# Kernel optimization log

Hardware: AMD Instinct MI355X
Metric: run time of the kernel (lower is better)

## Reference

```python
import jax, jax.numpy as jnp
import numpy as np

LATENT, HIDDEN = 512, 1024


def _gru_cell(x, h, w_ih, w_hh, b_ih, b_hh):
    # PyTorch GRU cell: gates ordered (r, z, n)
    gi = x @ w_ih.T + b_ih          # (B, 3H)
    gh = h @ w_hh.T + b_hh          # (B, 3H)
    i_r, i_z, i_n = jnp.split(gi, 3, axis=-1)
    h_r, h_z, h_n = jnp.split(gh, 3, axis=-1)
    r = jax.nn.sigmoid(i_r + h_r)
    z = jax.nn.sigmoid(i_z + h_z)
    n = jnp.tanh(i_n + r * h_n)
    return (1.0 - z) * n + z * h


def setup_inputs() -> dict:
    key = jax.random.key(0)
    ks = jax.random.split(key, 16)
    B, T_in = 128, 64
    k = 1.0 / np.sqrt(HIDDEN)
    u = lambda kk, shape: jax.random.uniform(kk, shape, jnp.float32, -k, k)
    return {
        "context_latents": jax.random.normal(ks[0], (B, T_in, LATENT), jnp.float32),
        "w_ih_l0": u(ks[1], (3 * HIDDEN, LATENT)),
        "w_hh_l0": u(ks[2], (3 * HIDDEN, HIDDEN)),
        "b_ih_l0": u(ks[3], (3 * HIDDEN,)),
        "b_hh_l0": u(ks[4], (3 * HIDDEN,)),
        "w_ih_l1": u(ks[5], (3 * HIDDEN, HIDDEN)),
        "w_hh_l1": u(ks[6], (3 * HIDDEN, HIDDEN)),
        "b_ih_l1": u(ks[7], (3 * HIDDEN,)),
        "b_hh_l1": u(ks[8], (3 * HIDDEN,)),
        "w1": u(ks[9], (HIDDEN, HIDDEN)),
        "bp1": u(ks[10], (HIDDEN,)),
        "w2": u(ks[11], (LATENT, HIDDEN)),
        "bp2": u(ks[12], (LATENT,)),
        "num_predictions": 64,
    }


def reference(context_latents, w_ih_l0, w_hh_l0, b_ih_l0, b_hh_l0,
              w_ih_l1, w_hh_l1, b_ih_l1, b_hh_l1, w1, bp1, w2, bp2,
              num_predictions):
    B = context_latents.shape[0]
    h0 = jnp.zeros((B, HIDDEN), context_latents.dtype)
    h1 = jnp.zeros((B, HIDDEN), context_latents.dtype)

    def stack(x_t, h0, h1):
        h0 = _gru_cell(x_t, h0, w_ih_l0, w_hh_l0, b_ih_l0, b_hh_l0)
        h1 = _gru_cell(h0, h1, w_ih_l1, w_hh_l1, b_ih_l1, b_hh_l1)
        return h0, h1

    # Encode context: scan over time (B, T_in, D) -> final hidden states
    def enc_step(carry, x_t):
        h0, h1 = carry
        h0, h1 = stack(x_t, h0, h1)
        return (h0, h1), None

    (h0, h1), _ = jax.lax.scan(enc_step, (h0, h1),
                               jnp.swapaxes(context_latents, 0, 1))

    def dec_step(carry, _):
        h0, h1, x = carry
        h0, h1 = stack(x, h0, h1)
        y = jax.nn.relu(h1 @ w1.T + bp1) @ w2.T + bp2   # (B, LATENT)
        return (h0, h1, y), y

    x0 = context_latents[:, -1, :]
    _, ys = jax.lax.scan(dec_step, (h0, h1, x0), None, length=num_predictions)
    return jnp.swapaxes(ys, 0, 1)  # (B, T_out, LATENT)
```

## Files before the change

kernel.cpp:

```cpp
#include <hip/hip_runtime.h>
#include <math.h>

#define B 128
#define LATENT 512
#define H 1024
#define BH (B * H)

typedef unsigned short ushort_t;
typedef unsigned int uint_t;
typedef __bf16 bf16x8 __attribute__((ext_vector_type(8)));
typedef float f32x4 __attribute__((ext_vector_type(4)));


__global__ __launch_bounds__(256) void zero4_kernel(float4* __restrict__ p, int n4) {
  int i = blockIdx.x * blockDim.x + threadIdx.x;
  int stride = gridDim.x * blockDim.x;
  float4 z = {0.f, 0.f, 0.f, 0.f};
  for (; i < n4; i += stride) p[i] = z;
}

__device__ __forceinline__ void split_bf16(float f, ushort_t& h, ushort_t& l) {
  uint_t u = __float_as_uint(f);
  uint_t hb = (u + 0x7FFFu + ((u >> 16) & 1u)) >> 16;
  float fh = __uint_as_float(hb << 16);
  float r = f - fh;
  uint_t v = __float_as_uint(r);
  uint_t lb = (v + 0x7FFFu + ((v >> 16) & 1u)) >> 16;
  h = (ushort_t)hb; l = (ushort_t)lb;
}

__global__ __launch_bounds__(256) void split_kernel(const float* __restrict__ src,
                                                    ushort_t* __restrict__ hi,
                                                    ushort_t* __restrict__ lo, int n) {
  int i = blockIdx.x * blockDim.x + threadIdx.x;
  int stride = gridDim.x * blockDim.x;
  for (; i < n; i += stride) {
    ushort_t h, l;
    split_bf16(src[i], h, l);
    hi[i] = h; lo[i] = l;
  }
}

__global__ __launch_bounds__(256) void split_hi_kernel(const float* __restrict__ src,
                                                       ushort_t* __restrict__ hi, int n) {
  int i = blockIdx.x * blockDim.x + threadIdx.x;
  int stride = gridDim.x * blockDim.x;
  for (; i < n; i += stride) {
    uint_t u = __float_as_uint(src[i]);
    hi[i] = (ushort_t)((u + 0x7FFFu + ((u >> 16) & 1u)) >> 16);
  }
}

__global__ __launch_bounds__(256) void wf_kernel(const float* __restrict__ wih0,
                                                 const float* __restrict__ w2,
                                                 ushort_t* __restrict__ wfh) {
  __shared__ float As[32][33];
  __shared__ float Bs[32][33];
  const int i0 = blockIdx.x * 32;
  const int k0 = blockIdx.y * 32;
  const int tid = threadIdx.x;
  const int r = tid >> 3, c4 = (tid & 7) << 2;
  float acc[4] = {0.f, 0.f, 0.f, 0.f};
  for (int m0 = 0; m0 < LATENT; m0 += 32) {
    {
      const float4 v = *reinterpret_cast<const float4*>(&wih0[(size_t)(i0 + r) * LATENT + m0 + c4]);
      As[r][c4] = v.x; As[r][c4 + 1] = v.y; As[r][c4 + 2] = v.z; As[r][c4 + 3] = v.w;
      const float4 w = *reinterpret_cast<const float4*>(&w2[(size_t)(m0 + r) * H + k0 + c4]);
      Bs[r][c4] = w.x; Bs[r][c4 + 1] = w.y; Bs[r][c4 + 2] = w.z; Bs[r][c4 + 3] = w.w;
    }
    __syncthreads();
    #pragma unroll
    for (int mm = 0; mm < 32; ++mm) {
      const float a = As[r][mm];
      #pragma unroll
      for (int x = 0; x < 4; ++x) acc[x] = fmaf(a, Bs[mm][c4 + x], acc[x]);
    }
    __syncthreads();
  }
  #pragma unroll
  for (int x = 0; x < 4; ++x) {
    uint_t u = __float_as_uint(acc[x]);
    wfh[(size_t)(i0 + r) * H + k0 + c4 + x] =
        (ushort_t)((u + 0x7FFFu + ((u >> 16) & 1u)) >> 16);
  }
}

__global__ __launch_bounds__(256) void bias_fuse_kernel(const float* __restrict__ wih0,
                                                        const float* __restrict__ bp2,
                                                        const float* __restrict__ bih0,
                                                        float* __restrict__ bf0) {
  int g = blockIdx.x * blockDim.x + threadIdx.x;
  if (g < 3 * H) {
    float s = bih0[g];
    const float* row = wih0 + (size_t)g * LATENT;
    #pragma unroll 4
    for (int l = 0; l < LATENT; ++l) s = fmaf(row[l], bp2[l], s);
    bf0[g] = s;
  }
}

__device__ __forceinline__ float sigmoidf_(float v) { return 1.0f / (1.0f + expf(-v)); }

__device__ __forceinline__ void grid_barrier(unsigned* bar, int tid, int bid) {
  __syncthreads();
  if (tid == 0) {
    const int g = bid & 7;
    unsigned* arr    = bar + (g << 6);
    unsigned* rel    = bar + 1024 + (g << 6);
    unsigned* master = bar + 2048;
    unsigned gen = __hip_atomic_load(rel, __ATOMIC_RELAXED, __HIP_MEMORY_SCOPE_AGENT);
    unsigned a = __hip_atomic_fetch_add(arr, 1u, __ATOMIC_ACQ_REL, __HIP_MEMORY_SCOPE_AGENT);
    if (a == 31u) {
      __hip_atomic_store(arr, 0u, __ATOMIC_RELAXED, __HIP_MEMORY_SCOPE_AGENT);
      unsigned m = __hip_atomic_fetch_add(master, 1u, __ATOMIC_ACQ_REL, __HIP_MEMORY_SCOPE_AGENT);
      if (m == 7u) {
        __hip_atomic_store(master, 0u, __ATOMIC_RELAXED, __HIP_MEMORY_SCOPE_AGENT);
        #pragma unroll
        for (int i = 0; i < 8; ++i)
          __hip_atomic_fetch_add(bar + 1024 + (i << 6), 1u, __ATOMIC_ACQ_REL, __HIP_MEMORY_SCOPE_AGENT);
      }
    }
    while (__hip_atomic_load(rel, __ATOMIC_RELAXED, __HIP_MEMORY_SCOPE_AGENT) == gen)
      __builtin_amdgcn_s_sleep(1);
    (void)__hip_atomic_load(rel, __ATOMIC_ACQUIRE, __HIP_MEMORY_SCOPE_AGENT);
  }
  __syncthreads();
}

template <int NJ, int NG, int PH, int EPI, bool WLO, int CHUNKW>
__device__ __forceinline__ void phase_mm(
    char* smem, const int tid, const int Mb, const int jb, const bool active,
    const ushort_t* aAh, const ushort_t* aAl, int aApitch, int K1,
    const ushort_t* wAh, const ushort_t* wAl,
    const ushort_t* aBh, const ushort_t* aBl, int aBpitch, int K2,
    const ushort_t* wBh,
    const float* bih, const float* bhh,
    const float* h_prev, float* h_out,
    ushort_t* out_hi, ushort_t* out_lo, int split_pitch,
    const float* bias, float* out_f32)
{
  if (!active) return;
  constexpr int KST = CHUNKW / 128;
  constexpr int SLOTB = CHUNKW * 32;
  constexpr int NW = NJ * NG;
  constexpr int NSLOTA = 4 + NW * (WLO ? 2 : 1);
  constexpr int NSLOTB = 4 + NW;
  constexpr int BUFB = NSLOTA * SLOTB;
  constexpr int NPG = PH * NW;
  constexpr int CW = NJ * 16;
  constexpr int CSHIFT = (CHUNKW == 256) ? 8 : 7;

  const int b0 = Mb * 32;
  const int j0 = jb * CW;
  const int NC1 = K1 >> CSHIFT;
  const int NC2 = (PH == 2) ? (K2 >> CSHIFT) : 0;
  const int NC = NC1 + NC2;

  const char* g[NSLOTA];
  auto build = [&](const ushort_t* ah, const ushort_t* al, int apitch,
                   const ushort_t* wh, const ushort_t* wl, int K) {
    const int rowt = tid >> 4;
    const int cp = tid & 15;
    const int cc = cp ^ rowt;
    #pragma unroll
    for (int u = 0; u < NSLOTA; ++u) {
      const ushort_t* basep; size_t off;
      if (u < 2)      { basep = ah; off = (size_t)(b0 + u * 16 + rowt) * apitch + cc * 8; }
      else if (u < 4) { basep = al; off = (size_t)(b0 + (u - 2) * 16 + rowt) * apitch + cc * 8; }
      else if (u < 4 + NW) {
        const int w = u - 4, jt = w % NJ, gate = w / NJ;
        const int wrow = (NG == 3) ? (gate * H + j0 + jt * 16 + rowt) : (j0 + jt * 16 + rowt);
        basep = wh; off = (size_t)wrow * K + cc * 8;
      } else {
        const int w = u - 4 - NW, jt = w % NJ, gate = w / NJ;
        const int wrow = (NG == 3) ? (gate * H + j0 + jt * 16 + rowt) : (j0 + jt * 16 + rowt);
        basep = (wl != nullptr) ? wl : wh; off = (size_t)wrow * K + cc * 8;
      }
      g[u] = (const char*)(basep + off);
    }
  };

  const int s = tid >> 6;
  const int q = (tid >> 4) & 3;
  const int r = tid & 15;
  int gsv[KST];
  #pragma unroll
  for (int k2 = 0; k2 < KST; ++k2) {
    const int G = s * (4 * KST) + k2 * 4 + q;
    gsv[k2] = (G >> 4) * 4096 + ((G & 15) ^ r) * 16;
  }
  const int rbase = r * 256;

  f32x4 accA[NJ][NG][2];
  f32x4 accB[NJ][NG][2];
  #pragma unroll
  for (int jt = 0; jt < NJ; ++jt)
    #pragma unroll
    for (int gg = 0; gg < NG; ++gg)
      #pragma unroll
      for (int mf = 0; mf < 2; ++mf) {
        accA[jt][gg][mf] = (f32x4){0.f, 0.f, 0.f, 0.f};
        accB[jt][gg][mf] = (f32x4){0.f, 0.f, 0.f, 0.f};
      }

  const unsigned wofs = (unsigned)(tid >> 6) * 1024;
  auto issue = [&](int bsel, int koff, int nslot) {
    #pragma unroll
    for (int u = 0; u < NSLOTA; ++u) {
      if (u < nslot) {
        #pragma unroll
        for (int j = 0; j < KST; ++j) {
          __builtin_amdgcn_global_load_lds(
              (const __attribute__((address_space(1))) void*)(g[u] + koff + j * 256),
              (__attribute__((address_space(3))) void*)(smem + bsel * BUFB + u * SLOTB + j * 4096 + wofs),
              16, 0, 0);
        }
      }
    }
  };

  auto computeA = [&](int bsel) {
    const char* base = smem + bsel * BUFB;
    #pragma unroll
    for (int k2 = 0; k2 < KST; ++k2) {
      const int fo = rbase + gsv[k2];
      bf16x8 ah0 = *(const bf16x8*)(base + 0 * SLOTB + fo);
      bf16x8 ah1 = *(const bf16x8*)(base + 1 * SLOTB + fo);
      bf16x8 al0 = *(const bf16x8*)(base + 2 * SLOTB + fo);
      bf16x8 al1 = *(const bf16x8*)(base + 3 * SLOTB + fo);
      #pragma unroll
      for (int gg = 0; gg < NG; ++gg)
        #pragma unroll
        for (int jt = 0; jt < NJ; ++jt) {
          const int w = gg * NJ + jt;
          bf16x8 wh = *(const bf16x8*)(base + (4 + w) * SLOTB + fo);
          accA[jt][gg][0] = __builtin_amdgcn_mfma_f32_16x16x32_bf16(ah0, wh, accA[jt][gg][0], 0, 0, 0);
          if (WLO) {
            bf16x8 wl = *(const bf16x8*)(base + (4 + NW + w) * SLOTB + fo);
            accA[jt][gg][0] = __builtin_amdgcn_mfma_f32_16x16x32_bf16(ah0, wl, accA[jt][gg][0], 0, 0, 0);
            accA[jt][gg][1] = __builtin_amdgcn_mfma_f32_16x16x32_bf16(ah1, wl, accA[jt][gg][1], 0, 0, 0);
          }
          accA[jt][gg][0] = __builtin_amdgcn_mfma_f32_16x16x32_bf16(al0, wh, accA[jt][gg][0], 0, 0, 0);
          accA[jt][gg][1] = __builtin_amdgcn_mfma_f32_16x16x32_bf16(ah1, wh, accA[jt][gg][1], 0, 0, 0);
          accA[jt][gg][1] = __builtin_amdgcn_mfma_f32_16x16x32_bf16(al1, wh, accA[jt][gg][1], 0, 0, 0);
        }
    }
  };
  auto computeB = [&](int bsel) {
    const char* base = smem + bsel * BUFB;
    #pragma unroll
    for (int k2 = 0; k2 < KST; ++k2) {
      const int fo = rbase + gsv[k2];
      bf16x8 ah0 = *(const bf16x8*)(base + 0 * SLOTB + fo);
      bf16x8 ah1 = *(const bf16x8*)(base + 1 * SLOTB + fo);
      bf16x8 al0 = *(const bf16x8*)(base + 2 * SLOTB + fo);
      bf16x8 al1 = *(const bf16x8*)(base + 3 * SLOTB + fo);
      #pragma unroll
      for (int gg = 0; gg < NG; ++gg)
        #pragma unroll
        for (int jt = 0; jt < NJ; ++jt) {
          const int w = gg * NJ + jt;
          bf16x8 wh = *(const bf16x8*)(base + (4 + w) * SLOTB + fo);
          accB[jt][gg][0] = __builtin_amdgcn_mfma_f32_16x16x32_bf16(ah0, wh, accB[jt][gg][0], 0, 0, 0);
          accB[jt][gg][0] = __builtin_amdgcn_mfma_f32_16x16x32_bf16(al0, wh, accB[jt][gg][0], 0, 0, 0);
          accB[jt][gg][1] = __builtin_amdgcn_mfma_f32_16x16x32_bf16(ah1, wh, accB[jt][gg][1], 0, 0, 0);
          accB[jt][gg][1] = __builtin_amdgcn_mfma_f32_16x16x32_bf16(al1, wh, accB[jt][gg][1], 0, 0, 0);
        }
    }
  };

  build(aAh, aAl, aApitch, wAh, wAl, K1);
  issue(0, 0, NSLOTA);

  #pragma unroll 1
  for (int c = 0; c < NC; ++c) {
    __syncthreads();
    if (c + 1 < NC) {
      if (PH == 2 && c + 1 == NC1) {
        build(aBh, aBl, aBpitch, wBh, nullptr, K2);
        issue((c + 1) & 1, 0, NSLOTB);
      } else {
        const bool isB = (PH == 2) && (c + 1 >= NC1);
        const int koff = (isB ? (c + 1 - NC1) : (c + 1)) * (CHUNKW * 2);
        issue((c + 1) & 1, koff, isB ? NSLOTB : NSLOTA);
      }
    }
    if (PH == 1 || c < NC1) computeA(c & 1);
    else                    computeB(c & 1);
  }
  __syncthreads();

  const int lane = tid & 63;
  #pragma unroll
  for (int gg = 0; gg < NG; ++gg)
    #pragma unroll
    for (int jt = 0; jt < NJ; ++jt)
      #pragma unroll
      for (int mf = 0; mf < 2; ++mf) {
        const int w = gg * NJ + jt;
        *(f32x4*)(smem + (size_t)(((s * NPG + w) * 2 + mf) * 64 + lane) * 16) = accA[jt][gg][mf];
        if (PH == 2)
          *(f32x4*)(smem + (size_t)(((s * NPG + NW + w) * 2 + mf) * 64 + lane) * 16) = accB[jt][gg][mf];
      }
  __syncthreads();

  for (int o = tid; o < 32 * CW; o += 256) {
    const int row = o / CW, c = o % CW;
    const int jt = c >> 4, cr = c & 15;
    const int mf = row >> 4, br = row & 15, qq = br >> 2, rg = br & 3;
    const int ln = cr + qq * 16;
    float v[PH * NG];
    #pragma unroll
    for (int pg = 0; pg < PH * NG; ++pg) {
      const int w = (pg < NG) ? (pg * NJ + jt) : (NW + (pg - NG) * NJ + jt);
      float sum = 0.f;
      #pragma unroll
      for (int ss = 0; ss < 4; ++ss)
        sum += *(const float*)(smem + (size_t)(((ss * NPG + w) * 2 + mf) * 64 + ln) * 16 + rg * 4);
      v[pg] = sum;
    }
    const int bglob = b0 + row, jglob = j0 + c;
    if (EPI == 0) {
      float ir = v[0] + bih[jglob];
      float iz = v[1] + bih[H + jglob];
      float in_ = v[2] + bih[2 * H + jglob];
      float hr = v[3] + bhh[jglob];
      float hz = v[4] + bhh[H + jglob];
      float hn = v[5] + bhh[2 * H + jglob];
      float rr_ = sigmoidf_(ir + hr);
      float zz_ = sigmoidf_(iz + hz);
      float nn_ = tanhf(in_ + rr_ * hn);
      float hp = h_prev[(size_t)bglob * H + jglob];
      float ho = (1.f - zz_) * nn_ + zz_ * hp;
      h_out[(size_t)bglob * H + jglob] = ho;
      ushort_t hb, lb;
      split_bf16(ho, hb, lb);
      out_hi[(size_t)bglob * H + jglob] = hb;
      out_lo[(size_t)bglob * H + jglob] = lb;
    } else if (EPI == 1) {
      float vv = v[0] + bias[jglob];
      vv = fmaxf(vv, 0.f);
      ushort_t hb, lb;
      split_bf16(vv, hb, lb);
      out_hi[(size_t)bglob * split_pitch + jglob] = hb;
      out_lo[(size_t)bglob * split_pitch + jglob] = lb;
    } else {
      float vv = v[0] + bias[jglob];
      const int tt = bglob >> 7, bb2 = bglob & 127;
      out_f32[((size_t)bb2 * split_pitch + tt) * LATENT + jglob] = vv;
    }
  }
  __syncthreads();
}


struct PParams {
  const ushort_t *ctxh, *ctxl;
  const ushort_t *wih0h, *whh0h;
  const ushort_t *wih1h, *whh1h;
  const ushort_t *w1h;
  const ushort_t *wfh;
  const float *bih0, *bhh0, *bih1, *bhh1, *bp1;
  const float *bf0;
  float *h0f0, *h0f1, *h1f0, *h1f1;
  ushort_t *h0hi0, *h0lo0, *h0hi1, *h0lo1;
  ushort_t *h1hi0, *h1lo0, *h1hi1, *h1lo1;
  ushort_t *h0Ahi, *h0Alo;
  unsigned* bar;
  int T_in, n_pred, ctx_pitch;
};

__global__ __launch_bounds__(256, 1) void gru_persistent(PParams P) {
  __shared__ char smem[114688];
  const int tid = threadIdx.x;
  const int bid = blockIdx.x;

  float* h0f[2] = {P.h0f0, P.h0f1};
  float* h1f[2] = {P.h1f0, P.h1f1};
  ushort_t* h0hi[2] = {P.h0hi0, P.h0hi1};
  ushort_t* h0lo[2] = {P.h0lo0, P.h0lo1};
  ushort_t* h1hi[2] = {P.h1hi0, P.h1hi1};
  ushort_t* h1lo[2] = {P.h1lo0, P.h1lo1};

  int p0 = 0, p1 = 0;

  const int idx = (bid < 128) ? bid : (bid - 128);
  const int eMb = idx & 3;
  const int ejb = idx >> 2;
  #pragma unroll 1
  for (int p = 0; p <= P.T_in; ++p) {
    const int n0 = p0 ^ 1, n1 = p1 ^ 1;
    if (bid < 128) {
      if (p < P.T_in) {
        const int t = p;
        phase_mm<2, 3, 2, 0, false, 128>(smem, tid, eMb, ejb, true,
            P.ctxh + (size_t)t * LATENT, P.ctxl + (size_t)t * LATENT, P.ctx_pitch, LATENT,
            P.wih0h, nullptr,
            (t == 0) ? P.h0hi0 : P.h0Ahi + (size_t)(t - 1) * BH,
            (t == 0) ? P.h0lo0 : P.h0Alo + (size_t)(t - 1) * BH, H, H, P.whh0h,
            P.bih0, P.bhh0, h0f[p0], h0f[n0],
            P.h0Ahi + (size_t)t * BH, P.h0Alo + (size_t)t * BH, H, nullptr, nullptr);
      }
    } else {
      if (p >= 1) {
        const int t = p - 1;
        phase_mm<2, 3, 2, 0, false, 128>(smem, tid, eMb, ejb, true,
            P.h0Ahi + (size_t)t * BH, P.h0Alo + (size_t)t * BH, H, H,
            P.wih1h, nullptr,
            h1hi[p1], h1lo[p1], H, H, P.whh1h,
            P.bih1, P.bhh1, h1f[p1], h1f[n1],
            h1hi[n1], h1lo[n1], H, nullptr, nullptr);
      }
    }
    grid_barrier(P.bar, tid, bid);
    if (p < P.T_in) p0 = n0;
    if (p >= 1) p1 = n1;
  }

  const int dMb = bid & 3;
  const int djb = bid >> 2;
  const ushort_t* d0ph = P.h0Ahi + (size_t)(P.T_in - 1) * BH;
  const ushort_t* d0pl = P.h0Alo + (size_t)(P.T_in - 1) * BH;
  ushort_t* pAh = P.h0Ahi;
  ushort_t* pAl = P.h0Alo;
  #pragma unroll 1
  for (int t = 0; t < P.n_pred; ++t) {
    const int n0 = p0 ^ 1;
    if (t == 0) {
      phase_mm<1, 3, 2, 0, false, 256>(smem, tid, dMb, djb, true,
          P.ctxh + (size_t)(P.T_in - 1) * LATENT, P.ctxl + (size_t)(P.T_in - 1) * LATENT,
          P.ctx_pitch, LATENT,
          P.wih0h, nullptr,
          d0ph, d0pl, H, H, P.whh0h,
          P.bih0, P.bhh0, h0f[p0], h0f[n0], h0hi[n0], h0lo[n0], H, nullptr, nullptr);
    } else {
      phase_mm<1, 3, 2, 0, false, 256>(smem, tid, dMb, djb, true,
          pAh + (size_t)(t - 1) * BH, pAl + (size_t)(t - 1) * BH, H, H,
          P.wfh, nullptr,
          d0ph, d0pl, H, H, P.whh0h,
          P.bf0, P.bhh0, h0f[p0], h0f[n0], h0hi[n0], h0lo[n0], H, nullptr, nullptr);
    }
    grid_barrier(P.bar, tid, bid);
    d0ph = h0hi[n0]; d0pl = h0lo[n0];
    const int n1 = p1 ^ 1;
    phase_mm<1, 3, 2, 0, false, 256>(smem, tid, dMb, djb, true,
        h0hi[n0], h0lo[n0], H, H,
        P.wih1h, nullptr,
        h1hi[p1], h1lo[p1], H, H, P.whh1h,
        P.bih1, P.bhh1, h1f[p1], h1f[n1], h1hi[n1], h1lo[n1], H, nullptr, nullptr);
    grid_barrier(P.bar, tid, bid);
    phase_mm<1, 1, 1, 1, false, 256>(smem, tid, dMb, djb, true,
        h1hi[n1], h1lo[n1], H, H,
        P.w1h, nullptr,
        nullptr, nullptr, 0, 0, nullptr,
        nullptr, nullptr, nullptr, nullptr,
        pAh + (size_t)t * BH, pAl + (size_t)t * BH, H, P.bp1, nullptr);
    grid_barrier(P.bar, tid, bid);
    p0 = n0; p1 = n1;
  }
}

__global__ __launch_bounds__(256, 2) void proj_out_kernel(
    const ushort_t* __restrict__ pAh, const ushort_t* __restrict__ pAl,
    const ushort_t* __restrict__ w2h, const float* __restrict__ bp2,
    float* __restrict__ out, int n_pred)
{
  __shared__ char smem[49152];
  const int tid = threadIdx.x;
  const int rt = blockIdx.x >> 4;
  const int ct = blockIdx.x & 15;
  phase_mm<2, 1, 1, 3, false, 128>(smem, tid, rt, ct, true,
      pAh, pAl, H, H,
      w2h, nullptr,
      nullptr, nullptr, 0, 0, nullptr,
      nullptr, nullptr, nullptr, nullptr,
      nullptr, nullptr, n_pred, bp2, out);
}


__global__ __launch_bounds__(256) void gru_cell_kernel(
    const float* __restrict__ x, int xs, int Kih,
    const float* __restrict__ h_prev,
    const float* __restrict__ wih, const float* __restrict__ whh,
    const float* __restrict__ bih, const float* __restrict__ bhh,
    float* __restrict__ h_out)
{
  __shared__ float Xs[32][33];
  __shared__ float Ws[48][33];
  const int tid = threadIdx.x;
  const int b0 = blockIdx.x * 32;
  const int j0 = blockIdx.y * 16;
  const int bg = tid & 15;
  const int jj = tid >> 4;
  const int j = j0 + jj;
  float accA[2][3];
  float accB[2][3];
  #pragma unroll
  for (int g = 0; g < 3; ++g) {
    const float bi = bih[g * H + j];
    const float bh = bhh[g * H + j];
    accA[0][g] = bi; accA[1][g] = bi;
    accB[0][g] = bh; accB[1][g] = bh;
  }
  for (int k0 = 0; k0 < Kih; k0 += 32) {
    {
      const int rr = tid >> 3, c4 = (tid & 7) << 2;
      const float4 v = *reinterpret_cast<const float4*>(&x[(size_t)(b0 + rr) * xs + k0 + c4]);
      Xs[rr][c4 + 0] = v.x; Xs[rr][c4 + 1] = v.y; Xs[rr][c4 + 2] = v.z; Xs[rr][c4 + 3] = v.w;
    }
    for (int li = tid; li < 48 * 8; li += 256) {
      const int rr = li >> 3, c4 = (li & 7) << 2;
      const int g = rr >> 4, jr = rr & 15;
      const float4 v = *reinterpret_cast<const float4*>(&wih[(size_t)(g * H + j0 + jr) * Kih + k0 + c4]);
      Ws[rr][c4 + 0] = v.x; Ws[rr][c4 + 1] = v.y; Ws[rr][c4 + 2] = v.z; Ws[rr][c4 + 3] = v.w;
    }
    __syncthreads();
    #pragma unroll
    for (int k = 0; k < 32; ++k) {
      const float x0 = Xs[bg][k];
      const float x1 = Xs[bg + 16][k];
      #pragma unroll
      for (int g = 0; g < 3; ++g) {
        const float wv = Ws[g * 16 + jj][k];
        accA[0][g] = fmaf(x0, wv, accA[0][g]);
        accA[1][g] = fmaf(x1, wv, accA[1][g]);
      }
    }
    __syncthreads();
  }
  for (int k0 = 0; k0 < H; k0 += 32) {
    {
      const int rr = tid >> 3, c4 = (tid & 7) << 2;
      const float4 v = *reinterpret_cast<const float4*>(&h_prev[(size_t)(b0 + rr) * H + k0 + c4]);
      Xs[rr][c4 + 0] = v.x; Xs[rr][c4 + 1] = v.y; Xs[rr][c4 + 2] = v.z; Xs[rr][c4 + 3] = v.w;
    }
    for (int li = tid; li < 48 * 8; li += 256) {
      const int rr = li >> 3, c4 = (li & 7) << 2;
      const int g = rr >> 4, jr = rr & 15;
      const float4 v = *reinterpret_cast<const float4*>(&whh[(size_t)(g * H + j0 + jr) * H + k0 + c4]);
      Ws[rr][c4 + 0] = v.x; Ws[rr][c4 + 1] = v.y; Ws[rr][c4 + 2] = v.z; Ws[rr][c4 + 3] = v.w;
    }
    __syncthreads();
    #pragma unroll
    for (int k = 0; k < 32; ++k) {
      const float h0v = Xs[bg][k];
      const float h1v = Xs[bg + 16][k];
      #pragma unroll
      for (int g = 0; g < 3; ++g) {
        const float wv = Ws[g * 16 + jj][k];
        accB[0][g] = fmaf(h0v, wv, accB[0][g]);
        accB[1][g] = fmaf(h1v, wv, accB[1][g]);
      }
    }
    __syncthreads();
  }
  #pragma unroll
  for (int i = 0; i < 2; ++i) {
    const int b = b0 + bg + i * 16;
    const float hp = h_prev[(size_t)b * H + j];
    const float r = sigmoidf_(accA[i][0] + accB[i][0]);
    const float z = sigmoidf_(accA[i][1] + accB[i][1]);
    const float n = tanhf(accA[i][2] + r * accB[i][2]);
    h_out[(size_t)b * H + j] = (1.0f - z) * n + z * hp;
  }
}

__global__ __launch_bounds__(256) void gemm_bias_kernel(
    const float* __restrict__ X, int xs, int K,
    const float* __restrict__ W, const float* __restrict__ bias,
    float* __restrict__ out1, int o1s,
    float* __restrict__ out2, int o2s,
    int relu)
{
  __shared__ float Xs[32][33];
  __shared__ float Ws[16][33];
  const int tid = threadIdx.x;
  const int b0 = blockIdx.x * 32;
  const int n0 = blockIdx.y * 16;
  const int bg = tid & 15;
  const int nn = tid >> 4;
  const int n = n0 + nn;
  float acc0 = bias[n];
  float acc1 = acc0;
  for (int k0 = 0; k0 < K; k0 += 32) {
    {
      const int rr = tid >> 3, c4 = (tid & 7) << 2;
      const float4 v = *reinterpret_cast<const float4*>(&X[(size_t)(b0 + rr) * xs + k0 + c4]);
      Xs[rr][c4 + 0] = v.x; Xs[rr][c4 + 1] = v.y; Xs[rr][c4 + 2] = v.z; Xs[rr][c4 + 3] = v.w;
    }
    if (tid < 128) {
      const int rr = tid >> 3, c4 = (tid & 7) << 2;
      const float4 v = *reinterpret_cast<const float4*>(&W[(size_t)(n0 + rr) * K + k0 + c4]);
      Ws[rr][c4 + 0] = v.x; Ws[rr][c4 + 1] = v.y; Ws[rr][c4 + 2] = v.z; Ws[rr][c4 + 3] = v.w;
    }
    __syncthreads();
    #pragma unroll
    for (int k = 0; k < 32; ++k) {
      const float wv = Ws[nn][k];
      acc0 = fmaf(Xs[bg][k], wv, acc0);
      acc1 = fmaf(Xs[bg + 16][k], wv, acc1);
    }
    __syncthreads();
  }
  if (relu) { acc0 = fmaxf(acc0, 0.0f); acc1 = fmaxf(acc1, 0.0f); }
  const int ba = b0 + bg, bb = b0 + bg + 16;
  out1[(size_t)ba * o1s + n] = acc0;
  out1[(size_t)bb * o1s + n] = acc1;
  if (out2 != nullptr) {
    out2[(size_t)ba * o2s + n] = acc0;
    out2[(size_t)bb * o2s + n] = acc1;
  }
}


extern "C" void kernel_launch(void* const* d_in, const int* in_sizes, int n_in,
                              void* d_out, int out_size, void* d_ws, size_t ws_size,
                              hipStream_t stream) {
  (void)n_in;
  const float* ctx  = (const float*)d_in[0];
  const float* wih0 = (const float*)d_in[1];
  const float* whh0 = (const float*)d_in[2];
  const float* bih0 = (const float*)d_in[3];
  const float* bhh0 = (const float*)d_in[4];
  const float* wih1 = (const float*)d_in[5];
  const float* whh1 = (const float*)d_in[6];
  const float* bih1 = (const float*)d_in[7];
  const float* bhh1 = (const float*)d_in[8];
  const float* w1   = (const float*)d_in[9];
  const float* bp1  = (const float*)d_in[10];
  const float* w2   = (const float*)d_in[11];
  const float* bp2  = (const float*)d_in[12];

  const int T_in   = in_sizes[0] / (B * LATENT);
  const int n_pred = out_size / (B * LATENT);
  float* out = (float*)d_out;

  size_t cur = 0;
  auto alloc = [&](size_t bytes) -> void* {
    void* p = (char*)d_ws + cur;
    cur += (bytes + 255) & ~(size_t)255;
    return p;
  };
  const int E_wih0 = 3 * H * LATENT, E_whh0 = 3 * H * H;
  const int E_wih1 = 3 * H * H, E_whh1 = 3 * H * H;
  const int E_w1 = H * H, E_w2 = LATENT * H;
  const int E_wf = 3 * H * H;
  const int E_ctx = in_sizes[0];

  ushort_t* wih0h = (ushort_t*)alloc(E_wih0 * 2);
  ushort_t* whh0h = (ushort_t*)alloc(E_whh0 * 2);
  ushort_t* wih1h = (ushort_t*)alloc(E_wih1 * 2);
  ushort_t* whh1h = (ushort_t*)alloc(E_whh1 * 2);
  ushort_t* w1h   = (ushort_t*)alloc(E_w1 * 2);
  ushort_t* w2h   = (ushort_t*)alloc(E_w2 * 2);
  ushort_t* wfh   = (ushort_t*)alloc((size_t)E_wf * 2);
  ushort_t* ctxh  = (ushort_t*)alloc((size_t)E_ctx * 2);
  ushort_t* ctxl  = (ushort_t*)alloc((size_t)E_ctx * 2);
  ushort_t* h0Ahi = (ushort_t*)alloc((size_t)T_in * BH * 2);
  ushort_t* h0Alo = (ushort_t*)alloc((size_t)T_in * BH * 2);
  float* bf0 = (float*)alloc(3 * H * 4);
  size_t zero_start = cur;
  float* h0f[2]; float* h1f[2];
  ushort_t* h0hi[2]; ushort_t* h0lo[2]; ushort_t* h1hi[2]; ushort_t* h1lo[2];
  h0f[0] = (float*)alloc(BH * 4); h0f[1] = (float*)alloc(BH * 4);
  h1f[0] = (float*)alloc(BH * 4); h1f[1] = (float*)alloc(BH * 4);
  h0hi[0] = (ushort_t*)alloc(BH * 2); h0lo[0] = (ushort_t*)alloc(BH * 2);
  h0hi[1] = (ushort_t*)alloc(BH * 2); h0lo[1] = (ushort_t*)alloc(BH * 2);
  h1hi[0] = (ushort_t*)alloc(BH * 2); h1lo[0] = (ushort_t*)alloc(BH * 2);
  h1hi[1] = (ushort_t*)alloc(BH * 2); h1lo[1] = (ushort_t*)alloc(BH * 2);
  unsigned* bar = (unsigned*)alloc(16384);
  size_t zero_bytes = cur - zero_start;
  size_t required = cur;

  if (ws_size >= required && n_pred <= T_in) {
    auto splitA = [&](const float* s, ushort_t* hi, ushort_t* lo, int n) {
      int blocks = (n + 255) / 256; if (blocks > 2048) blocks = 2048;
      split_kernel<<<blocks, 256, 0, stream>>>(s, hi, lo, n);
    };
    auto splitW = [&](const float* s, ushort_t* hi, int n) {
      int blocks = (n + 255) / 256; if (blocks > 2048) blocks = 2048;
      split_hi_kernel<<<blocks, 256, 0, stream>>>(s, hi, n);
    };
    splitW(wih0, wih0h, E_wih0);
    splitW(whh0, whh0h, E_whh0);
    splitW(wih1, wih1h, E_wih1);
    splitW(whh1, whh1h, E_whh1);
    splitW(w1, w1h, E_w1);
    splitW(w2, w2h, E_w2);
    wf_kernel<<<dim3(3 * H / 32, H / 32), 256, 0, stream>>>(wih0, w2, wfh);
    bias_fuse_kernel<<<(3 * H + 255) / 256, 256, 0, stream>>>(wih0, bp2, bih0, bf0);
    splitA(ctx, ctxh, ctxl, E_ctx);
    {
      int n4 = (int)(zero_bytes / 16);
      zero4_kernel<<<2048, 256, 0, stream>>>((float4*)((char*)d_ws + zero_start), n4);
    }

    PParams P;
    P.ctxh = ctxh; P.ctxl = ctxl;
    P.wih0h = wih0h; P.whh0h = whh0h;
    P.wih1h = wih1h; P.whh1h = whh1h;
    P.w1h = w1h; P.wfh = wfh;
    P.bih0 = bih0; P.bhh0 = bhh0; P.bih1 = bih1; P.bhh1 = bhh1; P.bp1 = bp1;
    P.bf0 = bf0;
    P.h0f0 = h0f[0]; P.h0f1 = h0f[1]; P.h1f0 = h1f[0]; P.h1f1 = h1f[1];
    P.h0hi0 = h0hi[0]; P.h0lo0 = h0lo[0]; P.h0hi1 = h0hi[1]; P.h0lo1 = h0lo[1];
    P.h1hi0 = h1hi[0]; P.h1lo0 = h1lo[0]; P.h1hi1 = h1hi[1]; P.h1lo1 = h1lo[1];
    P.h0Ahi = h0Ahi; P.h0Alo = h0Alo;
    P.bar = bar;
    P.T_in = T_in; P.n_pred = n_pred; P.ctx_pitch = T_in * LATENT;

    gru_persistent<<<256, 256, 0, stream>>>(P);

    const int rowtiles = (n_pred * B) / 32;
    proj_out_kernel<<<rowtiles * 16, 256, 0, stream>>>(h0Ahi, h0Alo, w2h, bp2, out, n_pred);
    return;
  }

  float* ws = (float*)d_ws;
  float* h0a = ws;
  float* h0b = h0a + (size_t)BH;
  float* h1a = h0b + (size_t)BH;
  float* h1b = h1a + (size_t)BH;
  float* p   = h1b + (size_t)BH;
  {
    int n4 = (4 * BH) / 4;
    zero4_kernel<<<256, 256, 0, stream>>>((float4*)h0a, n4);
  }
  float* y = p + (size_t)BH;
  float* h0p = h0a; float* h0n = h0b;
  float* h1p = h1a; float* h1n = h1b;
  const dim3 cgrid(4, 64);
  for (int t = 0; t < T_in; ++t) {
    const float* x = ctx + (size_t)t * LATENT;
    gru_cell_kernel<<<cgrid, 256, 0, stream>>>(x, T_in * LATENT, LATENT,
                                               h0p, wih0, whh0, bih0, bhh0, h0n);
    gru_cell_kernel<<<cgrid, 256, 0, stream>>>(h0n, H, H,
                                               h1p, wih1, whh1, bih1, bhh1, h1n);
    float* tmp;
    tmp = h0p; h0p = h0n; h0n = tmp;
    tmp = h1p; h1p = h1n; h1n = tmp;
  }
  for (int t = 0; t < n_pred; ++t) {
    const float* x; int xstride;
    if (t == 0) { x = ctx + (size_t)(T_in - 1) * LATENT; xstride = T_in * LATENT; }
    else        { x = y; xstride = LATENT; }
    gru_cell_kernel<<<cgrid, 256, 0, stream>>>(x, xstride, LATENT,
                                               h0p, wih0, whh0, bih0, bhh0, h0n);
    gru_cell_kernel<<<cgrid, 256, 0, stream>>>(h0n, H, H,
                                               h1p, wih1, whh1, bih1, bhh1, h1n);
    gemm_bias_kernel<<<dim3(4, H / 16), 256, 0, stream>>>(h1n, H, H, w1, bp1,
                                                          p, H, nullptr, 0, 1);
    gemm_bias_kernel<<<dim3(4, LATENT / 16), 256, 0, stream>>>(p, H, H, w2, bp2,
                                                               y, LATENT,
                                                               out + (size_t)t * LATENT,
                                                               n_pred * LATENT, 0);
    float* tmp;
    tmp = h0p; h0p = h0n; h0n = tmp;
    tmp = h1p; h1p = h1n; h1n = tmp;
  }
}
```

Before: 6.560 ms.

## Relax grid barrier ordering and load activations via coherent atomics through registers

The grid barrier's acquire/release atomics become relaxed, and the trailing acquire load is dropped. To keep cross-block data visible without those fences, the activation tiles that change every step are now read with relaxed agent-scope atomic loads into registers and written to LDS after compute, which overlaps them with the MFMA work. Weight tiles still use async global-to-LDS loads. Epilogue stores of hidden state and split outputs become relaxed atomic stores. This removes cache flush and invalidate costs at each barrier, but memory ordering now depends on relaxed atomics. It also adds register pressure and possible visibility bugs.

```diff
diff --git a/kernel.cpp b/kernel.cpp
--- a/kernel.cpp
+++ b/kernel.cpp
@@ -10,6 +10,9 @@
 typedef unsigned int uint_t;
 typedef __bf16 bf16x8 __attribute__((ext_vector_type(8)));
 typedef float f32x4 __attribute__((ext_vector_type(4)));
+
+#define AT_LD(p)    __hip_atomic_load((p), __ATOMIC_RELAXED, __HIP_MEMORY_SCOPE_AGENT)
+#define AT_ST(p, v) __hip_atomic_store((p), (v), __ATOMIC_RELAXED, __HIP_MEMORY_SCOPE_AGENT)
 
 
 __global__ __launch_bounds__(256) void zero4_kernel(float4* __restrict__ p, int n4) {
@@ -108,21 +111,20 @@
     unsigned* arr    = bar + (g << 6);
     unsigned* rel    = bar + 1024 + (g << 6);
     unsigned* master = bar + 2048;
-    unsigned gen = __hip_atomic_load(rel, __ATOMIC_RELAXED, __HIP_MEMORY_SCOPE_AGENT);
-    unsigned a = __hip_atomic_fetch_add(arr, 1u, __ATOMIC_ACQ_REL, __HIP_MEMORY_SCOPE_AGENT);
+    unsigned gen = AT_LD(rel);
+    unsigned a = __hip_atomic_fetch_add(arr, 1u, __ATOMIC_RELAXED, __HIP_MEMORY_SCOPE_AGENT);
     if (a == 31u) {
-      __hip_atomic_store(arr, 0u, __ATOMIC_RELAXED, __HIP_MEMORY_SCOPE_AGENT);
-      unsigned m = __hip_atomic_fetch_add(master, 1u, __ATOMIC_ACQ_REL, __HIP_MEMORY_SCOPE_AGENT);
+      AT_ST(arr, 0u);
+      unsigned m = __hip_atomic_fetch_add(master, 1u, __ATOMIC_RELAXED, __HIP_MEMORY_SCOPE_AGENT);
       if (m == 7u) {
-        __hip_atomic_store(master, 0u, __ATOMIC_RELAXED, __HIP_MEMORY_SCOPE_AGENT);
+        AT_ST(master, 0u);
         #pragma unroll
         for (int i = 0; i < 8; ++i)
-          __hip_atomic_fetch_add(bar + 1024 + (i << 6), 1u, __ATOMIC_ACQ_REL, __HIP_MEMORY_SCOPE_AGENT);
-      }
-    }
-    while (__hip_atomic_load(rel, __ATOMIC_RELAXED, __HIP_MEMORY_SCOPE_AGENT) == gen)
+          __hip_atomic_fetch_add(bar + 1024 + (i << 6), 1u, __ATOMIC_RELAXED, __HIP_MEMORY_SCOPE_AGENT);
+      }
+    }
+    while (AT_LD(rel) == gen)
       __builtin_amdgcn_s_sleep(1);
-    (void)__hip_atomic_load(rel, __ATOMIC_ACQUIRE, __HIP_MEMORY_SCOPE_AGENT);
   }
   __syncthreads();
 }
@@ -204,9 +206,9 @@
       }
 
   const unsigned wofs = (unsigned)(tid >> 6) * 1024;
-  auto issue = [&](int bsel, int koff, int nslot) {
-    #pragma unroll
-    for (int u = 0; u < NSLOTA; ++u) {
+  auto issueW = [&](int bsel, int koff, int nslot) {
+    #pragma unroll
+    for (int u = 4; u < NSLOTA; ++u) {
       if (u < nslot) {
         #pragma unroll
         for (int j = 0; j < KST; ++j) {
@@ -217,6 +219,27 @@
         }
       }
     }
+  };
+
+  uint4 aReg[4][KST];
+  auto loadA = [&](int koff) {
+    #pragma unroll
+    for (int u = 0; u < 4; ++u)
+      #pragma unroll
+      for (int j = 0; j < KST; ++j) {
+        uint_t* p = (uint_t*)(void*)(g[u] + koff + j * 256);
+        aReg[u][j].x = AT_LD(p + 0);
+        aReg[u][j].y = AT_LD(p + 1);
+        aReg[u][j].z = AT_LD(p + 2);
+        aReg[u][j].w = AT_LD(p + 3);
+      }
+  };
+  auto writeA = [&](int bsel) {
+    #pragma unroll
+    for (int u = 0; u < 4; ++u)
+      #pragma unroll
+      for (int j = 0; j < KST; ++j)
+        *(uint4*)(smem + bsel * BUFB + u * SLOTB + j * 4096 + tid * 16) = aReg[u][j];
   };
 
   auto computeA = [&](int bsel) {
@@ -270,7 +293,9 @@
   };
 
   build(aAh, aAl, aApitch, wAh, wAl, K1);
-  issue(0, 0, NSLOTA);
+  issueW(0, 0, NSLOTA);
+  loadA(0);
+  writeA(0);
 
   #pragma unroll 1
   for (int c = 0; c < NC; ++c) {
@@ -278,15 +303,18 @@
     if (c + 1 < NC) {
       if (PH == 2 && c + 1 == NC1) {
         build(aBh, aBl, aBpitch, wBh, nullptr, K2);
-        issue((c + 1) & 1, 0, NSLOTB);
+        issueW((c + 1) & 1, 0, NSLOTB);
+        loadA(0);
       } else {
         const bool isB = (PH == 2) && (c + 1 >= NC1);
         const int koff = (isB ? (c + 1 - NC1) : (c + 1)) * (CHUNKW * 2);
-        issue((c + 1) & 1, koff, isB ? NSLOTB : NSLOTA);
+        issueW((c + 1) & 1, koff, isB ? NSLOTB : NSLOTA);
+        loadA(koff);
       }
     }
     if (PH == 1 || c < NC1) computeA(c & 1);
     else                    computeB(c & 1);
+    if (c + 1 < NC) writeA((c + 1) & 1);
   }
   __syncthreads();
 
@@ -330,20 +358,20 @@
       float rr_ = sigmoidf_(ir + hr);
       float zz_ = sigmoidf_(iz + hz);
       float nn_ = tanhf(in_ + rr_ * hn);
-      float hp = h_prev[(size_t)bglob * H + jglob];
+      float hp = AT_LD((float*)&h_prev[(size_t)bglob * H + jglob]);
       float ho = (1.f - zz_) * nn_ + zz_ * hp;
-      h_out[(size_t)bglob * H + jglob] = ho;
+      AT_ST(&h_out[(size_t)bglob * H + jglob], ho);
       ushort_t hb, lb;
       split_bf16(ho, hb, lb);
-      out_hi[(size_t)bglob * H + jglob] = hb;
-      out_lo[(size_t)bglob * H + jglob] = lb;
+      AT_ST(&out_hi[(size_t)bglob * H + jglob], hb);
+      AT_ST(&out_lo[(size_t)bglob * H + jglob], lb);
     } else if (EPI == 1) {
       float vv = v[0] + bias[jglob];
       vv = fmaxf(vv, 0.f);
       ushort_t hb, lb;
       split_bf16(vv, hb, lb);
-      out_hi[(size_t)bglob * split_pitch + jglob] = hb;
-      out_lo[(size_t)bglob * split_pitch + jglob] = lb;
+      AT_ST(&out_hi[(size_t)bglob * split_pitch + jglob], hb);
+      AT_ST(&out_lo[(size_t)bglob * split_pitch + jglob], lb);
     } else {
       float vv = v[0] + bias[jglob];
       const int tt = bglob >> 7, bb2 = bglob & 127;
```

Result: slower. 6.929 ms (+5.6%).
